# Kernel tuning notes

Hardware: AMD Instinct MI355X
Metric: run time of the kernel (lower is better)

## Reference

```python
import jax, jax.numpy as jnp
import numpy as np

B, C, H, W = 4, 256, 128, 128
OUT = 50

def setup_inputs() -> dict:
    key = jax.random.key(0)
    k1, k2, k3 = jax.random.split(key, 3)
    x = jax.random.normal(k1, (B, C, H, W), dtype=jnp.float32)
    # conv2d 1x1 weights, kaiming-ish scale
    W_f = jax.random.normal(k2, (OUT, C), dtype=jnp.float32) * (1.0 / np.sqrt(C))
    W_beta = jax.random.normal(k3, (C, C), dtype=jnp.float32) * (1.0 / np.sqrt(C))
    return {"x": x, "W_f": W_f, "W_beta": W_beta}

def reference(x, W_f, W_beta):
    b, c, h, w = x.shape
    n = h * w
    xf = x.reshape(b, c, n)                      # [B,C,N]
    F = jnp.einsum('oc,bcn->bon', W_f, xf)       # 1x1 conv -> [B,O,N]
    # S = softmax(F @ A, axis over C), A = xf^T : [B,N,C]
    S = jnp.einsum('bon,bcn->boc', F, xf)        # [B,O,C]
    S = jax.nn.softmax(S, axis=2)
    St = jnp.swapaxes(S, 1, 2)                   # [B,C,O]
    E = jnp.einsum('bco,bon->bcn', St, F)        # [B,C,N]
    E = E.reshape(b, c, h, w)
    E = jnp.einsum('dc,bchw->bdhw', W_beta, E) + x  # beta conv + residual
    return E
```

## Files before the change

kernel.cpp:

```cpp
#include <hip/hip_runtime.h>
#include <math.h>

#define CCH 256
#define OCH 50
#define NPIX 16384
#define BATCH 4
#define BO (BATCH*OCH)
#define NSPLIT2 128
#define KC2 (NPIX/NSPLIT2)

typedef _Float16 f16x8 __attribute__((ext_vector_type(8)));
typedef float f32x4 __attribute__((ext_vector_type(4)));

__device__ __forceinline__ void cvt_split(const float4 v0, const float4 v1,
                                          f16x8& h, f16x8& l) {
    float v[8] = {v0.x, v0.y, v0.z, v0.w, v1.x, v1.y, v1.z, v1.w};
#pragma unroll
    for (int j = 0; j < 8; ++j) {
        _Float16 hj = (_Float16)v[j];
        h[j] = hj;
        l[j] = (_Float16)(v[j] - (float)hj);
    }
}

__global__ void k0_transpose(const float* __restrict__ Wf, float* __restrict__ WfT) {
    int i = blockIdx.x * 256 + threadIdx.x;
    if (i < OCH * CCH) {
        int o = i / CCH, c = i % CCH;
        WfT[c * OCH + o] = Wf[i];
    }
}

__global__ __launch_bounds__(256) void k1_F(const float* __restrict__ x,
                                            const float* __restrict__ WfT,
                                            float* __restrict__ F) {
    const int OH = 25;
    int b  = blockIdx.y;
    int oh = blockIdx.z;
    int n  = blockIdx.x * 256 + threadIdx.x;
    float acc[OH];
#pragma unroll
    for (int j = 0; j < OH; ++j) acc[j] = 0.f;
    const float* xp = x + (size_t)b * CCH * NPIX + n;
    const float* wp = WfT + oh * OH;
    for (int c = 0; c < CCH; c += 4) {
        float x0 = xp[(size_t)(c + 0) * NPIX];
        float x1 = xp[(size_t)(c + 1) * NPIX];
        float x2 = xp[(size_t)(c + 2) * NPIX];
        float x3 = xp[(size_t)(c + 3) * NPIX];
        const float* w0 = wp + (c + 0) * OCH;
        const float* w1 = wp + (c + 1) * OCH;
        const float* w2 = wp + (c + 2) * OCH;
        const float* w3 = wp + (c + 3) * OCH;
#pragma unroll
        for (int j = 0; j < OH; ++j) {
            acc[j] = fmaf(w0[j], x0, acc[j]);
            acc[j] = fmaf(w1[j], x1, acc[j]);
            acc[j] = fmaf(w2[j], x2, acc[j]);
            acc[j] = fmaf(w3[j], x3, acc[j]);
        }
    }
    float* Fp = F + ((size_t)b * 64 + oh * OH) * NPIX + n;
#pragma unroll
    for (int j = 0; j < OH; ++j) Fp[(size_t)j * NPIX] = acc[j];
}

__global__ __launch_bounds__(256) void k2_mfma(const float* __restrict__ x,
                                               const float* __restrict__ F,
                                               float* __restrict__ Spart) {
    int ks = blockIdx.x;
    int b  = blockIdx.y;
    int wave = threadIdx.x >> 6;
    int lane = threadIdx.x & 63;
    int r16  = lane & 15;
    int kg   = lane >> 4;
    int n0   = ks * KC2;

    f32x4 acc[16];
#pragma unroll
    for (int nt = 0; nt < 16; ++nt) acc[nt] = {0.f, 0.f, 0.f, 0.f};

    const float* Ab = F + ((size_t)b * 64 + wave * 16 + r16) * NPIX + n0 + kg * 8;
    const float* Bb = x + ((size_t)b * CCH + r16) * NPIX + n0 + kg * 8;

#pragma unroll
    for (int kk = 0; kk < KC2 / 32; ++kk) {
        const float* ap = Ab + kk * 32;
        f16x8 ah, al;
        cvt_split(*(const float4*)ap, *(const float4*)(ap + 4), ah, al);
#pragma unroll
        for (int nt = 0; nt < 16; ++nt) {
            const float* bp = Bb + (size_t)nt * 16 * NPIX + kk * 32;
            f16x8 bh, bl;
            cvt_split(*(const float4*)bp, *(const float4*)(bp + 4), bh, bl);
            acc[nt] = __builtin_amdgcn_mfma_f32_16x16x32_f16(ah, bh, acc[nt], 0, 0, 0);
            acc[nt] = __builtin_amdgcn_mfma_f32_16x16x32_f16(ah, bl, acc[nt], 0, 0, 0);
            acc[nt] = __builtin_amdgcn_mfma_f32_16x16x32_f16(al, bh, acc[nt], 0, 0, 0);
        }
    }
    float* Sp = Spart + (((size_t)ks * BATCH + b) * 64 + wave * 16 + kg * 4) * 256 + r16;
#pragma unroll
    for (int nt = 0; nt < 16; ++nt)
#pragma unroll
        for (int r = 0; r < 4; ++r)
            Sp[(size_t)r * 256 + nt * 16] = acc[nt][r];
}

__global__ __launch_bounds__(1024) void k2r_softmax(const float* __restrict__ Spart,
                                                    float* __restrict__ S) {
    int row = blockIdx.x;
    int b = row / OCH, o = row % OCH;
    int tid = threadIdx.x;
    int c = tid & 255, g = tid >> 8;
    __shared__ float part[4][CCH];
    __shared__ float red[8];
    float v = 0.f;
    const size_t ksStride = (size_t)BATCH * 64 * 256;
    const float* p = Spart + ((size_t)(g * (NSPLIT2 / 4)) * BATCH + b) * 64 * 256
                   + (size_t)o * 256 + c;
#pragma unroll 8
    for (int ks = 0; ks < NSPLIT2 / 4; ++ks)
        v += p[ks * ksStride];
    part[g][c] = v;
    __syncthreads();
    float vv = 0.f, e = 0.f, m;
    if (tid < 256) {
        vv = part[0][c] + part[1][c] + part[2][c] + part[3][c];
        m = vv;
#pragma unroll
        for (int off = 32; off > 0; off >>= 1) m = fmaxf(m, __shfl_xor(m, off, 64));
        if ((tid & 63) == 0) red[tid >> 6] = m;
    }
    __syncthreads();
    if (tid < 256) {
        m = fmaxf(fmaxf(red[0], red[1]), fmaxf(red[2], red[3]));
        e = expf(vv - m);
        float s = e;
#pragma unroll
        for (int off = 32; off > 0; off >>= 1) s += __shfl_xor(s, off, 64);
        if ((tid & 63) == 0) red[4 + (tid >> 6)] = s;
    }
    __syncthreads();
    if (tid < 256) {
        float tot = red[4] + red[5] + red[6] + red[7];
        S[(size_t)row * CCH + c] = e / tot;
    }
}

__global__ __launch_bounds__(256) void k3_M(const float* __restrict__ Wbeta,
                                            const float* __restrict__ S,
                                            float* __restrict__ Mt) {
    int row = blockIdx.x;
    int d = threadIdx.x;
    const float* srow = S + (size_t)row * CCH;
    const float4* wb = (const float4*)(Wbeta + (size_t)d * CCH);
    float acc = 0.f;
#pragma unroll 4
    for (int cg = 0; cg < CCH / 4; ++cg) {
        float4 w = wb[cg];
        float4 s = *(const float4*)(srow + cg * 4);
        acc += w.x * s.x + w.y * s.y + w.z * s.z + w.w * s.w;
    }
    Mt[(size_t)row * CCH + d] = acc;
}

__global__ __launch_bounds__(256) void k4_out(const float* __restrict__ x,
                                              const float* __restrict__ F,
                                              const float* __restrict__ Mt,
                                              float* __restrict__ out) {
    int b  = blockIdx.z;
    int dq = blockIdx.y;
    int n  = blockIdx.x * 256 + threadIdx.x;
    float acc[64];
#pragma unroll
    for (int dd = 0; dd < 64; ++dd) acc[dd] = 0.f;
    const float* Fp = F + (size_t)b * 64 * NPIX + n;
    const float* mt = Mt + (size_t)b * OCH * CCH + dq * 64;
#pragma unroll 2
    for (int o = 0; o < OCH; ++o) {
        float fo = Fp[(size_t)o * NPIX];
        const float* m = mt + o * CCH;
#pragma unroll
        for (int dd = 0; dd < 64; ++dd) acc[dd] = fmaf(m[dd], fo, acc[dd]);
    }
    const float* xp = x + ((size_t)b * CCH + dq * 64) * NPIX + n;
    float* op = out + ((size_t)b * CCH + dq * 64) * NPIX + n;
#pragma unroll
    for (int dd = 0; dd < 64; ++dd)
        __builtin_nontemporal_store(acc[dd] + xp[(size_t)dd * NPIX], &op[(size_t)dd * NPIX]);
}

extern "C" void kernel_launch(void* const* d_in, const int* in_sizes, int n_in,
                              void* d_out, int out_size, void* d_ws, size_t ws_size,
                              hipStream_t stream) {
    const float* x     = (const float*)d_in[0];
    const float* Wf    = (const float*)d_in[1];
    const float* Wbeta = (const float*)d_in[2];
    float* out = (float*)d_out;

    float* F   = (float*)d_ws;
    float* WfT = F + (size_t)BATCH * 64 * NPIX;
    float* S   = WfT + CCH * OCH;
    float* Mt  = S + (size_t)BO * CCH;
    float* Spart = out;

    k0_transpose<<<dim3((OCH * CCH + 255) / 256), dim3(256), 0, stream>>>(Wf, WfT);
    k1_F<<<dim3(NPIX / 256, BATCH, 2), dim3(256), 0, stream>>>(x, WfT, F);
    k2_mfma<<<dim3(NSPLIT2, BATCH), dim3(256), 0, stream>>>(x, F, Spart);
    k2r_softmax<<<dim3(BO), dim3(1024), 0, stream>>>(Spart, S);
    k3_M<<<dim3(BO), dim3(256), 0, stream>>>(Wbeta, S, Mt);
    k4_out<<<dim3(NPIX / 256, 4, BATCH), dim3(256), 0, stream>>>(x, F, Mt, out);
}
```

Baseline: 242.3 us.

## Compute F with split-fp16 MFMA and widen k2/k4 grids

Replaces the scalar-FMA 1x1 conv kernel producing F with an MFMA kernel. It pre-packs W_f into hi/lo fp16 pairs and stages x tiles through swizzled, double-buffered LDS as packed hi/lo fp16, using three MFMAs per tile to keep near-fp32 accuracy. It also splits the S-partial MFMA kernel over two channel halves and the output kernel over eight channel groups instead of four, raising block count and lowering per-thread accumulator pressure. The cost is extra conversion work and LDS traffic, plus more redundant reads of F in k4.

```diff
diff --git a/kernel.cpp b/kernel.cpp
--- a/kernel.cpp
+++ b/kernel.cpp
@@ -11,6 +11,8 @@
 
 typedef _Float16 f16x8 __attribute__((ext_vector_type(8)));
 typedef float f32x4 __attribute__((ext_vector_type(4)));
+typedef unsigned int uint;
+typedef unsigned short ushort;
 
 __device__ __forceinline__ void cvt_split(const float4 v0, const float4 v1,
                                           f16x8& h, f16x8& l) {
@@ -23,46 +25,100 @@
     }
 }
 
-__global__ void k0_transpose(const float* __restrict__ Wf, float* __restrict__ WfT) {
+__device__ __forceinline__ uint packhl(float v) {
+    _Float16 h = (_Float16)v;
+    _Float16 l = (_Float16)(v - (float)h);
+    union { _Float16 f; ushort u; } H, L;
+    H.f = h; L.f = l;
+    return (uint)H.u | ((uint)L.u << 16);
+}
+
+__device__ __forceinline__ void unpack8(const uint* w, f16x8& h, f16x8& l) {
+    union { uint u[4]; f16x8 v; } H, L;
+#pragma unroll
+    for (int k = 0; k < 4; ++k) {
+        H.u[k] = __builtin_amdgcn_perm(w[2 * k + 1], w[2 * k], 0x05040100u);
+        L.u[k] = __builtin_amdgcn_perm(w[2 * k + 1], w[2 * k], 0x07060302u);
+    }
+    h = H.v; l = L.v;
+}
+
+__global__ void k0_pack(const float* __restrict__ Wf, uint* __restrict__ Wf16p) {
     int i = blockIdx.x * 256 + threadIdx.x;
-    if (i < OCH * CCH) {
-        int o = i / CCH, c = i % CCH;
-        WfT[c * OCH + o] = Wf[i];
-    }
-}
-
-__global__ __launch_bounds__(256) void k1_F(const float* __restrict__ x,
-                                            const float* __restrict__ WfT,
-                                            float* __restrict__ F) {
-    const int OH = 25;
+    if (i < 64 * CCH) {
+        int o = i / CCH;
+        float v = (o < OCH) ? Wf[i] : 0.f;
+        Wf16p[i] = packhl(v);
+    }
+}
+
+__global__ __launch_bounds__(256) void k1_mfma(const float* __restrict__ x,
+                                               const uint* __restrict__ Wf16p,
+                                               float* __restrict__ F) {
     int b  = blockIdx.y;
-    int oh = blockIdx.z;
-    int n  = blockIdx.x * 256 + threadIdx.x;
-    float acc[OH];
-#pragma unroll
-    for (int j = 0; j < OH; ++j) acc[j] = 0.f;
-    const float* xp = x + (size_t)b * CCH * NPIX + n;
-    const float* wp = WfT + oh * OH;
-    for (int c = 0; c < CCH; c += 4) {
-        float x0 = xp[(size_t)(c + 0) * NPIX];
-        float x1 = xp[(size_t)(c + 1) * NPIX];
-        float x2 = xp[(size_t)(c + 2) * NPIX];
-        float x3 = xp[(size_t)(c + 3) * NPIX];
-        const float* w0 = wp + (c + 0) * OCH;
-        const float* w1 = wp + (c + 1) * OCH;
-        const float* w2 = wp + (c + 2) * OCH;
-        const float* w3 = wp + (c + 3) * OCH;
-#pragma unroll
-        for (int j = 0; j < OH; ++j) {
-            acc[j] = fmaf(w0[j], x0, acc[j]);
-            acc[j] = fmaf(w1[j], x1, acc[j]);
-            acc[j] = fmaf(w2[j], x2, acc[j]);
-            acc[j] = fmaf(w3[j], x3, acc[j]);
-        }
-    }
-    float* Fp = F + ((size_t)b * 64 + oh * OH) * NPIX + n;
-#pragma unroll
-    for (int j = 0; j < OH; ++j) Fp[(size_t)j * NPIX] = acc[j];
+    int p0 = blockIdx.x * 64;
+    int t  = threadIdx.x;
+    int w = t >> 6, lane = t & 63, r16 = lane & 15, kg = lane >> 4;
+    __shared__ uint xl[2][32 * 64];
+
+    int cidx = t & 15;
+    int pixg = t >> 4;
+    const float* xb = x + ((size_t)b * CCH) * NPIX + p0;
+
+    float4 r0 = *(const float4*)(xb + (size_t)cidx * NPIX + pixg * 4);
+    float4 r1 = *(const float4*)(xb + (size_t)(16 + cidx) * NPIX + pixg * 4);
+
+    f32x4 acc[4];
+#pragma unroll
+    for (int nt = 0; nt < 4; ++nt) acc[nt] = {0.f, 0.f, 0.f, 0.f};
+
+    const uint* Arow = Wf16p + (w * 16 + r16) * CCH;
+
+#pragma unroll
+    for (int s = 0; s < 8; ++s) {
+        uint* buf = xl[s & 1];
+        float v0[4] = {r0.x, r0.y, r0.z, r0.w};
+        float v1[4] = {r1.x, r1.y, r1.z, r1.w};
+#pragma unroll
+        for (int j = 0; j < 4; ++j) {
+            int pix = pixg * 4 + j;
+            int q = (pix & 7) << 2;
+            buf[pix * 32 + (cidx ^ q)]        = packhl(v0[j]);
+            buf[pix * 32 + ((16 + cidx) ^ q)] = packhl(v1[j]);
+        }
+        if (s < 7) {
+            r0 = *(const float4*)(xb + (size_t)((s + 1) * 32 + cidx) * NPIX + pixg * 4);
+            r1 = *(const float4*)(xb + (size_t)((s + 1) * 32 + 16 + cidx) * NPIX + pixg * 4);
+        }
+        __syncthreads();
+
+        uint aw[8];
+        *(uint4*)aw       = *(const uint4*)(Arow + s * 32 + kg * 8);
+        *(uint4*)(aw + 4) = *(const uint4*)(Arow + s * 32 + kg * 8 + 4);
+        f16x8 Ah, Al;
+        unpack8(aw, Ah, Al);
+
+#pragma unroll
+        for (int nt = 0; nt < 4; ++nt) {
+            int pix = nt * 16 + r16;
+            int q = (r16 & 7) << 2;
+            uint bw[8];
+            *(uint4*)bw       = *(const uint4*)&buf[pix * 32 + ((kg * 8) ^ q)];
+            *(uint4*)(bw + 4) = *(const uint4*)&buf[pix * 32 + ((kg * 8 + 4) ^ q)];
+            f16x8 Bh, Bl;
+            unpack8(bw, Bh, Bl);
+            acc[nt] = __builtin_amdgcn_mfma_f32_16x16x32_f16(Ah, Bh, acc[nt], 0, 0, 0);
+            acc[nt] = __builtin_amdgcn_mfma_f32_16x16x32_f16(Ah, Bl, acc[nt], 0, 0, 0);
+            acc[nt] = __builtin_amdgcn_mfma_f32_16x16x32_f16(Al, Bh, acc[nt], 0, 0, 0);
+        }
+    }
+
+    float* Fb = F + ((size_t)b * 64 + w * 16 + kg * 4) * NPIX + p0;
+#pragma unroll
+    for (int nt = 0; nt < 4; ++nt)
+#pragma unroll
+        for (int r = 0; r < 4; ++r)
+            Fb[(size_t)r * NPIX + nt * 16 + r16] = acc[nt][r];
 }
 
 __global__ __launch_bounds__(256) void k2_mfma(const float* __restrict__ x,
@@ -70,18 +126,19 @@
                                                float* __restrict__ Spart) {
     int ks = blockIdx.x;
     int b  = blockIdx.y;
+    int ch = blockIdx.z;
     int wave = threadIdx.x >> 6;
     int lane = threadIdx.x & 63;
     int r16  = lane & 15;
     int kg   = lane >> 4;
     int n0   = ks * KC2;
 
-    f32x4 acc[16];
-#pragma unroll
-    for (int nt = 0; nt < 16; ++nt) acc[nt] = {0.f, 0.f, 0.f, 0.f};
+    f32x4 acc[8];
+#pragma unroll
+    for (int nt = 0; nt < 8; ++nt) acc[nt] = {0.f, 0.f, 0.f, 0.f};
 
     const float* Ab = F + ((size_t)b * 64 + wave * 16 + r16) * NPIX + n0 + kg * 8;
-    const float* Bb = x + ((size_t)b * CCH + r16) * NPIX + n0 + kg * 8;
+    const float* Bb = x + ((size_t)b * CCH + ch * 128 + r16) * NPIX + n0 + kg * 8;
 
 #pragma unroll
     for (int kk = 0; kk < KC2 / 32; ++kk) {
@@ -89,7 +146,7 @@
         f16x8 ah, al;
         cvt_split(*(const float4*)ap, *(const float4*)(ap + 4), ah, al);
 #pragma unroll
-        for (int nt = 0; nt < 16; ++nt) {
+        for (int nt = 0; nt < 8; ++nt) {
             const float* bp = Bb + (size_t)nt * 16 * NPIX + kk * 32;
             f16x8 bh, bl;
             cvt_split(*(const float4*)bp, *(const float4*)(bp + 4), bh, bl);
@@ -98,9 +155,10 @@
             acc[nt] = __builtin_amdgcn_mfma_f32_16x16x32_f16(al, bh, acc[nt], 0, 0, 0);
         }
     }
-    float* Sp = Spart + (((size_t)ks * BATCH + b) * 64 + wave * 16 + kg * 4) * 256 + r16;
-#pragma unroll
-    for (int nt = 0; nt < 16; ++nt)
+    float* Sp = Spart + (((size_t)ks * BATCH + b) * 64 + wave * 16 + kg * 4) * 256
+              + ch * 128 + r16;
+#pragma unroll
+    for (int nt = 0; nt < 8; ++nt)
 #pragma unroll
         for (int r = 0; r < 4; ++r)
             Sp[(size_t)r * 256 + nt * 16] = acc[nt][r];
@@ -171,22 +229,22 @@
     int b  = blockIdx.z;
     int dq = blockIdx.y;
     int n  = blockIdx.x * 256 + threadIdx.x;
-    float acc[64];
-#pragma unroll
-    for (int dd = 0; dd < 64; ++dd) acc[dd] = 0.f;
+    float acc[32];
+#pragma unroll
+    for (int dd = 0; dd < 32; ++dd) acc[dd] = 0.f;
     const float* Fp = F + (size_t)b * 64 * NPIX + n;
-    const float* mt = Mt + (size_t)b * OCH * CCH + dq * 64;
+    const float* mt = Mt + (size_t)b * OCH * CCH + dq * 32;
 #pragma unroll 2
     for (int o = 0; o < OCH; ++o) {
         float fo = Fp[(size_t)o * NPIX];
         const float* m = mt + o * CCH;
 #pragma unroll
-        for (int dd = 0; dd < 64; ++dd) acc[dd] = fmaf(m[dd], fo, acc[dd]);
-    }
-    const float* xp = x + ((size_t)b * CCH + dq * 64) * NPIX + n;
-    float* op = out + ((size_t)b * CCH + dq * 64) * NPIX + n;
-#pragma unroll
-    for (int dd = 0; dd < 64; ++dd)
+        for (int dd = 0; dd < 32; ++dd) acc[dd] = fmaf(m[dd], fo, acc[dd]);
+    }
+    const float* xp = x + ((size_t)b * CCH + dq * 32) * NPIX + n;
+    float* op = out + ((size_t)b * CCH + dq * 32) * NPIX + n;
+#pragma unroll
+    for (int dd = 0; dd < 32; ++dd)
         __builtin_nontemporal_store(acc[dd] + xp[(size_t)dd * NPIX], &op[(size_t)dd * NPIX]);
 }
 
@@ -198,16 +256,16 @@
     const float* Wbeta = (const float*)d_in[2];
     float* out = (float*)d_out;
 
-    float* F   = (float*)d_ws;
-    float* WfT = F + (size_t)BATCH * 64 * NPIX;
-    float* S   = WfT + CCH * OCH;
-    float* Mt  = S + (size_t)BO * CCH;
+    float* F     = (float*)d_ws;
+    uint*  Wf16p = (uint*)(F + (size_t)BATCH * 64 * NPIX);
+    float* S     = (float*)(Wf16p + 64 * CCH);
+    float* Mt    = S + (size_t)BO * CCH;
     float* Spart = out;
 
-    k0_transpose<<<dim3((OCH * CCH + 255) / 256), dim3(256), 0, stream>>>(Wf, WfT);
-    k1_F<<<dim3(NPIX / 256, BATCH, 2), dim3(256), 0, stream>>>(x, WfT, F);
-    k2_mfma<<<dim3(NSPLIT2, BATCH), dim3(256), 0, stream>>>(x, F, Spart);
+    k0_pack<<<dim3((64 * CCH + 255) / 256), dim3(256), 0, stream>>>(Wf, Wf16p);
+    k1_mfma<<<dim3(NPIX / 64, BATCH), dim3(256), 0, stream>>>(x, Wf16p, F);
+    k2_mfma<<<dim3(NSPLIT2, BATCH, 2), dim3(256), 0, stream>>>(x, F, Spart);
     k2r_softmax<<<dim3(BO), dim3(1024), 0, stream>>>(Spart, S);
     k3_M<<<dim3(BO), dim3(256), 0, stream>>>(Wbeta, S, Mt);
-    k4_out<<<dim3(NPIX / 256, 4, BATCH), dim3(256), 0, stream>>>(x, F, Mt, out);
-}
+    k4_out<<<dim3(NPIX / 256, 8, BATCH), dim3(256), 0, stream>>>(x, F, Mt, out);
+}
```

After: 202.8 us. 16.3% less time.
